# Performance work log

Hardware: AMD Instinct MI355X
Metric: run time of the kernel (lower is better)

## Reference

```python
import jax, jax.numpy as jnp
import numpy as np

N_HEAD = 16
N_KV = 4
ROT = 128  # rotary_dim == head_dim
BASE = 10000
N_CTX = 1024


def make_sincos(n_ctx, rotary_dim, base):
    # GPT-NeoX style (rotary_adjacent_pairs=False): freq repeated twice
    pos = jnp.arange(n_ctx, dtype=jnp.float32)
    dim = jnp.arange(rotary_dim // 2, dtype=jnp.float32)
    freq = jnp.float32(base) ** (dim / (rotary_dim / 2))
    freq = jnp.tile(freq, 2)  # [rotary_dim]
    angles = pos[:, None] / freq[None, :]  # [n_ctx, rotary_dim]
    return jnp.sin(angles), jnp.cos(angles)


def setup_inputs() -> dict:
    key = jax.random.key(0)
    ks = jax.random.split(key, 5)
    B, T, C = 8, 1024, 2048
    r = N_HEAD // N_KV
    Ckv = C // r
    s = 0.02
    x = jax.random.normal(ks[0], (B, T, C), jnp.float32)
    wq = jax.random.normal(ks[1], (C, C), jnp.float32) * s
    wk = jax.random.normal(ks[2], (C, Ckv), jnp.float32) * s
    wv = jax.random.normal(ks[3], (C, Ckv), jnp.float32) * s
    wo = jax.random.normal(ks[4], (C, C), jnp.float32) * s
    sin, cos = make_sincos(N_CTX, ROT, BASE)
    return dict(x=x, wq=wq, wk=wk, wv=wv, wo=wo, sin=sin, cos=cos)


def _rope(x, sin, cos):
    # x: [B, H, T, hd]; rotary applied to first ROT dims (here ROT == hd)
    T = x.shape[2]
    n = ROT // 2
    x_rot = x[..., :ROT]
    x_pass = x[..., ROT:]
    # rotate_every_two (NeoX style): [x0..x_{n-1}, x_n..] -> [-x_n.., x0..]
    x_flip = jnp.concatenate([-x_rot[..., n:], x_rot[..., :n]], axis=-1)
    c = cos[None, None, :T, :]
    s = sin[None, None, :T, :]
    x_rotated = x_rot * c + x_flip * s
    return jnp.concatenate([x_rotated, x_pass], axis=-1)


def reference(x, wq, wk, wv, wo, sin, cos):
    B, T, C = x.shape
    H = N_HEAD
    hd = C // H
    r = H // N_KV
    q = (x @ wq).reshape(B, T, H, hd).transpose(0, 2, 1, 3)  # [B,H,T,hd]
    # Original: repeat_interleave along seq dim then view(B,T,H,hd).
    # Equivalent to tiling the kv channel vector r times per position.
    k = jnp.tile(x @ wk, (1, 1, r)).reshape(B, T, H, hd).transpose(0, 2, 1, 3)
    v = jnp.tile(x @ wv, (1, 1, r)).reshape(B, T, H, hd).transpose(0, 2, 1, 3)
    q = _rope(q, sin, cos)
    k = _rope(k, sin, cos)
    att = jnp.einsum('bhqd,bhkd->bhqk', q, k) / jnp.sqrt(jnp.float32(hd))
    causal = jnp.tril(jnp.ones((T, T), dtype=bool))
    att = jnp.where(causal[None, None], att, -jnp.inf)
    att = jax.nn.softmax(att, axis=-1)
    y = jnp.einsum('bhqk,bhkd->bhqd', att, v)
    y = y.transpose(0, 2, 1, 3).reshape(B, T, C)
    return y @ wo
```

## Files before the change

### kernel.cpp

```cpp
#include <hip/hip_runtime.h>

typedef __attribute__((ext_vector_type(8))) short short8;
typedef __attribute__((ext_vector_type(4))) float f32x4;

#define B_    8
#define T_    1024
#define C_    2048
#define H_    16
#define HKV_  4
#define HD_   128
#define M_    8192
#define NQKV_ 3072
#define KDIM_ 2048

__device__ __forceinline__ unsigned short f2bf(float f) {
  unsigned u = __float_as_uint(f);
  u += 0x7FFF + ((u >> 16) & 1);
  return (unsigned short)(u >> 16);
}
__device__ __forceinline__ float bf2f(unsigned short h) {
  return __uint_as_float(((unsigned)h) << 16);
}

__device__ __forceinline__ void async16(const unsigned short* g, unsigned short* l) {
  __builtin_amdgcn_global_load_lds(
      (const unsigned int __attribute__((address_space(1)))*)g,
      (unsigned int __attribute__((address_space(3)))*)l,
      16, 0, 0);
}

__global__ __launch_bounds__(256) void cvt_bf16_kernel(const float* __restrict__ in,
                                                       unsigned short* __restrict__ out) {
  int idx = blockIdx.x * 256 + threadIdx.x;
  float4 v = ((const float4*)in)[idx];
  ushort4 o;
  o.x = f2bf(v.x); o.y = f2bf(v.y); o.z = f2bf(v.z); o.w = f2bf(v.w);
  ((ushort4*)out)[idx] = o;
}

__global__ __launch_bounds__(256) void tpose_f32_bf16(const float* __restrict__ in,
                                                      unsigned short* __restrict__ out,
                                                      int Cc, int ldo) {
  __shared__ unsigned short tile[32][33];
  int c0 = blockIdx.x * 32, r0 = blockIdx.y * 32;
  int tx = threadIdx.x, ty = threadIdx.y;
#pragma unroll
  for (int j = 0; j < 4; j++)
    tile[ty + j * 8][tx] = f2bf(in[(size_t)(r0 + ty + j * 8) * Cc + c0 + tx]);
  __syncthreads();
#pragma unroll
  for (int j = 0; j < 4; j++)
    out[(size_t)(c0 + ty + j * 8) * ldo + r0 + tx] = tile[tx][ty + j * 8];
}

__global__ __launch_bounds__(256) void vtpose(const unsigned short* __restrict__ qkv,
                                              unsigned short* __restrict__ vt) {
  __shared__ unsigned short tile[32][33];
  int b = blockIdx.z;
  int c0 = blockIdx.x * 32, t0 = blockIdx.y * 32;
  int tx = threadIdx.x, ty = threadIdx.y;
  const unsigned short* src = qkv + (size_t)b * T_ * NQKV_ + 2560;
#pragma unroll
  for (int j = 0; j < 4; j++)
    tile[ty + j * 8][tx] = src[(size_t)(t0 + ty + j * 8) * NQKV_ + c0 + tx];
  __syncthreads();
  unsigned short* dst = vt + (size_t)b * 512 * T_;
#pragma unroll
  for (int j = 0; j < 4; j++)
    dst[(size_t)(c0 + ty + j * 8) * T_ + t0 + tx] = tile[tx][ty + j * 8];
}

__global__ __launch_bounds__(256) void rope_kernel(const unsigned short* __restrict__ qkv,
                                                   const float* __restrict__ sinp,
                                                   const float* __restrict__ cosp,
                                                   unsigned short* __restrict__ qatt,
                                                   unsigned short* __restrict__ katt) {
  int m = blockIdx.x;
  int b = m >> 10, t = m & 1023;
  int tid = threadIdx.x;
  int d = tid & 63;
  const unsigned short* row = qkv + (size_t)m * NQKV_;
  float c0 = cosp[t * 128 + d], s0 = sinp[t * 128 + d];
  float c1 = cosp[t * 128 + d + 64], s1 = sinp[t * 128 + d + 64];
#pragma unroll
  for (int h0 = 0; h0 < 16; h0 += 4) {
    int h = h0 + (tid >> 6);
    float x0 = bf2f(row[h * 128 + d]);
    float x1 = bf2f(row[h * 128 + d + 64]);
    size_t o = ((size_t)(b * 16 + h) * 1024 + t) * 128 + d;
    qatt[o]      = f2bf(x0 * c0 - x1 * s0);
    qatt[o + 64] = f2bf(x1 * c1 + x0 * s1);
  }
  {
    int kh = tid >> 6;
    float x0 = bf2f(row[2048 + kh * 128 + d]);
    float x1 = bf2f(row[2048 + kh * 128 + d + 64]);
    size_t o = ((size_t)(b * 4 + kh) * 1024 + t) * 128 + d;
    katt[o]      = f2bf(x0 * c0 - x1 * s0);
    katt[o + 64] = f2bf(x1 * c1 + x0 * s1);
  }
}

template <int OUTF32>
__global__ __launch_bounds__(512, 2) void gemm_v2(const unsigned short* __restrict__ A,
                                                  const unsigned short* __restrict__ BT,
                                                  void* __restrict__ Cout, int N) {
  __shared__ __align__(16) unsigned short lA[2][256 * 64];
  __shared__ __align__(16) unsigned short lB[2][128 * 64];
  const int K = KDIM_;
  int tid = threadIdx.x;
  int lane = tid & 63;
  int w = tid >> 6;
  int quad = lane >> 4, l16 = lane & 15;
  int wm = w >> 1, wn = w & 1;
  int gx = gridDim.x;
  int nwg = gx * gridDim.y;
  int lin = blockIdx.y * gx + blockIdx.x;
  int cpx = nwg >> 3;
  int swz = (lin & 7) * cpx + (lin >> 3);
  int bm = swz / gx, bn = swz % gx;
  const unsigned short* Ab = A + (size_t)bm * 256 * K;
  const unsigned short* Bb = BT + (size_t)bn * 128 * K;
  int klin = (tid & 7) * 8;
  int arow[4], acol[4];
#pragma unroll
  for (int j = 0; j < 4; j++) {
    int r = (j * 512 + tid) >> 3;
    arow[j] = r;
    acol[j] = klin ^ (((r >> 2) & 3) * 16);
  }
  int brow[2], bcol[2];
#pragma unroll
  for (int j = 0; j < 2; j++) {
    int r = (j * 512 + tid) >> 3;
    brow[j] = r;
    bcol[j] = klin ^ (((r >> 2) & 3) * 16);
  }
  const int rsw = ((l16 >> 2) & 3) * 16;
  f32x4 acc[4][4] = {};
#pragma unroll
  for (int j = 0; j < 4; j++)
    async16(Ab + (size_t)arow[j] * K + acol[j], &lA[0][(j * 512 + tid) * 8]);
#pragma unroll
  for (int j = 0; j < 2; j++)
    async16(Bb + (size_t)brow[j] * K + bcol[j], &lB[0][(j * 512 + tid) * 8]);
  asm volatile("s_waitcnt vmcnt(0)" ::: "memory");
  __builtin_amdgcn_s_barrier();
  int cur = 0;
  for (int kt = 0; kt < 32; kt++) {
    const unsigned short* pA = lA[cur];
    const unsigned short* pB = lB[cur];
    short8 af[2][2], bfr[4][2];
#pragma unroll
    for (int mt = 0; mt < 2; mt++)
#pragma unroll
      for (int ks = 0; ks < 2; ks++)
        af[mt][ks] = *(const short8*)&pA[(wm * 64 + mt * 16 + l16) * 64 +
                                         ((ks * 32 + quad * 8) ^ rsw)];
#pragma unroll
    for (int nt = 0; nt < 4; nt++)
#pragma unroll
      for (int ks = 0; ks < 2; ks++)
        bfr[nt][ks] = *(const short8*)&pB[(wn * 64 + nt * 16 + l16) * 64 +
                                          ((ks * 32 + quad * 8) ^ rsw)];
    if (kt < 31) {
      int k0 = (kt + 1) * 64;
#pragma unroll
      for (int j = 0; j < 4; j++)
        async16(Ab + (size_t)arow[j] * K + k0 + acol[j], &lA[cur ^ 1][(j * 512 + tid) * 8]);
#pragma unroll
      for (int j = 0; j < 2; j++)
        async16(Bb + (size_t)brow[j] * K + k0 + bcol[j], &lB[cur ^ 1][(j * 512 + tid) * 8]);
    }
    __builtin_amdgcn_s_barrier();
    __builtin_amdgcn_s_setprio(1);
#pragma unroll
    for (int mt = 0; mt < 2; mt++)
#pragma unroll
      for (int nt = 0; nt < 4; nt++)
#pragma unroll
        for (int ks = 0; ks < 2; ks++)
          acc[mt][nt] = __builtin_amdgcn_mfma_f32_16x16x32_bf16(af[mt][ks], bfr[nt][ks],
                                                                acc[mt][nt], 0, 0, 0);
    __builtin_amdgcn_s_setprio(0);
    __builtin_amdgcn_s_barrier();
    short8 ag[2][2];
#pragma unroll
    for (int mt = 0; mt < 2; mt++)
#pragma unroll
      for (int ks = 0; ks < 2; ks++)
        ag[mt][ks] = *(const short8*)&pA[(wm * 64 + (mt + 2) * 16 + l16) * 64 +
                                         ((ks * 32 + quad * 8) ^ rsw)];
    __builtin_amdgcn_s_setprio(1);
#pragma unroll
    for (int mt = 0; mt < 2; mt++)
#pragma unroll
      for (int nt = 0; nt < 4; nt++)
#pragma unroll
        for (int ks = 0; ks < 2; ks++)
          acc[mt + 2][nt] = __builtin_amdgcn_mfma_f32_16x16x32_bf16(ag[mt][ks], bfr[nt][ks],
                                                                    acc[mt + 2][nt], 0, 0, 0);
    __builtin_amdgcn_s_setprio(0);
    asm volatile("s_waitcnt vmcnt(0)" ::: "memory");
    __builtin_amdgcn_s_barrier();
    cur ^= 1;
  }
#pragma unroll
  for (int mt = 0; mt < 4; mt++) {
#pragma unroll
    for (int nt = 0; nt < 4; nt++) {
      int n = bn * 128 + wn * 64 + nt * 16 + l16;
#pragma unroll
      for (int r = 0; r < 4; r++) {
        int m = bm * 256 + wm * 64 + mt * 16 + quad * 4 + r;
        if (OUTF32)
          ((float*)Cout)[(size_t)m * N + n] = acc[mt][nt][r];
        else
          ((unsigned short*)Cout)[(size_t)m * N + n] = f2bf(acc[mt][nt][r]);
      }
    }
  }
}

__global__ __launch_bounds__(256, 2) void attn_kernel(const unsigned short* __restrict__ Q,
                                                      const unsigned short* __restrict__ Km,
                                                      const unsigned short* __restrict__ Vt,
                                                      unsigned short* __restrict__ Y) {
  __shared__ __align__(16) unsigned short lK[2][8192];
  __shared__ __align__(16) unsigned short lV[2][8192];
  __shared__ __align__(16) unsigned short lP[4608];
  int tid = threadIdx.x;
  int lane = tid & 63, w = tid >> 6;
  int quad = lane >> 4, l16 = lane & 15;
  int pq = blockIdx.x;
  int bh = blockIdx.y;
  int b = bh >> 4, h = bh & 15, kh = h & 3;
  const unsigned short* Kb = Km + (size_t)(b * 4 + kh) * T_ * 128;
  const unsigned short* Vb = Vt + (size_t)(b * 4 + kh) * 128 * T_;
  const float sc = 0.12751744690989f;
  unsigned short* pb = &lP[w * 1152];
  const int sw = (l16 & 3) * 8;

  int krow[4], kcol[4], vrow[4], vcol[4];
#pragma unroll
  for (int j = 0; j < 4; j++) {
    int i = tid + j * 256;
    int tq = (i & 3) ^ ((i >> 2) & 3);
    krow[j] = (i >> 2) & 63;
    kcol[j] = (i >> 8) * 32 + tq * 8;
    vrow[j] = (i >> 2) & 127;
    vcol[j] = (i >> 9) * 32 + tq * 8;
  }

  for (int ph = 0; ph < 2; ph++) {
    int qt = ph ? pq : 7 - pq;
    int qrow0 = qt * 128 + w * 32;
    const unsigned short* Qb = Q + ((size_t)bh * T_ + qrow0) * 128;
    short8 qf[2][4];
#pragma unroll
    for (int mt = 0; mt < 2; mt++)
#pragma unroll
      for (int ks = 0; ks < 4; ks++)
        qf[mt][ks] = *(const short8*)&Qb[(mt * 16 + l16) * 128 + ks * 32 + quad * 8];
    f32x4 o[2][8] = {};
    float m_r[2][4], l_r[2][4];
#pragma unroll
    for (int mt = 0; mt < 2; mt++)
#pragma unroll
      for (int r = 0; r < 4; r++) {
        m_r[mt][r] = -1e30f;
        l_r[mt][r] = 0.f;
      }
    int ntile = 2 * qt + 2;

    if (ph) __syncthreads();
#pragma unroll
    for (int j = 0; j < 4; j++)
      async16(Kb + (size_t)krow[j] * 128 + kcol[j], &lK[0][(tid + j * 256) * 8]);
#pragma unroll
    for (int j = 0; j < 4; j++)
      async16(Vb + (size_t)vrow[j] * T_ + vcol[j], &lV[0][(tid + j * 256) * 8]);
    asm volatile("s_waitcnt vmcnt(0)" ::: "memory");
    __syncthreads();

    int cur = 0;
    for (int kt = 0; kt < ntile; kt++) {
      int n0 = kt * 64;
      if (kt + 1 < ntile) {
        int n1 = n0 + 64;
#pragma unroll
        for (int j = 0; j < 4; j++)
          async16(Kb + (size_t)(n1 + krow[j]) * 128 + kcol[j], &lK[cur ^ 1][(tid + j * 256) * 8]);
#pragma unroll
        for (int j = 0; j < 4; j++)
          async16(Vb + (size_t)vrow[j] * T_ + n1 + vcol[j], &lV[cur ^ 1][(tid + j * 256) * 8]);
      }
      const unsigned short* lKc = lK[cur];
      const unsigned short* lVc = lV[cur];
      f32x4 s[2][4] = {};
      __builtin_amdgcn_s_setprio(1);
#pragma unroll
      for (int ct = 0; ct < 4; ct++) {
        short8 kf[4];
#pragma unroll
        for (int ks = 0; ks < 4; ks++)
          kf[ks] = *(const short8*)&lKc[ks * 2048 + (ct * 16 + l16) * 32 + (quad * 8 ^ sw)];
#pragma unroll
        for (int ks = 0; ks < 4; ks++) {
          s[0][ct] = __builtin_amdgcn_mfma_f32_16x16x32_bf16(qf[0][ks], kf[ks], s[0][ct], 0, 0, 0);
          s[1][ct] = __builtin_amdgcn_mfma_f32_16x16x32_bf16(qf[1][ks], kf[ks], s[1][ct], 0, 0, 0);
        }
      }
      __builtin_amdgcn_s_setprio(0);
      if (kt >= 2 * qt) {
#pragma unroll
        for (int mt = 0; mt < 2; mt++)
#pragma unroll
          for (int ct = 0; ct < 4; ct++) {
            int n = n0 + ct * 16 + l16;
#pragma unroll
            for (int r = 0; r < 4; r++) {
              int q = qrow0 + mt * 16 + quad * 4 + r;
              if (n > q) s[mt][ct][r] = -1e30f;
            }
          }
      }
      float alpha[2][4], msc[2][4];
#pragma unroll
      for (int mt = 0; mt < 2; mt++)
#pragma unroll
        for (int r = 0; r < 4; r++) {
          float v = fmaxf(fmaxf(s[mt][0][r], s[mt][1][r]), fmaxf(s[mt][2][r], s[mt][3][r]));
#pragma unroll
          for (int off = 1; off < 16; off <<= 1)
            v = fmaxf(v, __shfl_xor(v, off));
          float mn = fmaxf(m_r[mt][r], v);
          alpha[mt][r] = exp2f((m_r[mt][r] - mn) * sc);
          m_r[mt][r] = mn;
          msc[mt][r] = mn * sc;
        }
#pragma unroll
      for (int mt = 0; mt < 2; mt++)
#pragma unroll
        for (int ct = 0; ct < 4; ct++)
#pragma unroll
          for (int r = 0; r < 4; r++)
            s[mt][ct][r] = exp2f(fmaf(s[mt][ct][r], sc, -msc[mt][r]));
#pragma unroll
      for (int ct = 0; ct < 4; ct++)
#pragma unroll
        for (int r = 0; r < 4; r++)
          pb[(quad * 4 + r) * 72 + ct * 16 + l16] = f2bf(s[0][ct][r]);
#pragma unroll
      for (int mt = 0; mt < 2; mt++)
#pragma unroll
        for (int r = 0; r < 4; r++)
          l_r[mt][r] = l_r[mt][r] * alpha[mt][r] +
                       (s[mt][0][r] + s[mt][1][r]) + (s[mt][2][r] + s[mt][3][r]);
      bool needr = false;
#pragma unroll
      for (int mt = 0; mt < 2; mt++)
#pragma unroll
        for (int r = 0; r < 4; r++)
          needr |= (alpha[mt][r] != 1.0f);
      if (__any(needr)) {
#pragma unroll
        for (int mt = 0; mt < 2; mt++)
#pragma unroll
          for (int dt = 0; dt < 8; dt++)
#pragma unroll
            for (int r = 0; r < 4; r++)
              o[mt][dt][r] *= alpha[mt][r];
      }
      __builtin_amdgcn_s_waitcnt(0xC07F);
      short8 pa0[2];
#pragma unroll
      for (int ks2 = 0; ks2 < 2; ks2++)
        pa0[ks2] = *(const short8*)&pb[l16 * 72 + ks2 * 32 + quad * 8];
      __builtin_amdgcn_s_waitcnt(0xC07F);
      asm volatile("" ::: "memory");
#pragma unroll
      for (int ct = 0; ct < 4; ct++)
#pragma unroll
        for (int r = 0; r < 4; r++)
          pb[(quad * 4 + r) * 72 + ct * 16 + l16] = f2bf(s[1][ct][r]);
      __builtin_amdgcn_s_waitcnt(0xC07F);
      short8 pa1[2];
#pragma unroll
      for (int ks2 = 0; ks2 < 2; ks2++)
        pa1[ks2] = *(const short8*)&pb[l16 * 72 + ks2 * 32 + quad * 8];
      __builtin_amdgcn_s_setprio(1);
#pragma unroll
      for (int dt = 0; dt < 8; dt++) {
#pragma unroll
        for (int ks2 = 0; ks2 < 2; ks2++) {
          short8 vf = *(const short8*)&lVc[ks2 * 4096 + (dt * 16 + l16) * 32 + (quad * 8 ^ sw)];
          o[0][dt] = __builtin_amdgcn_mfma_f32_16x16x32_bf16(pa0[ks2], vf, o[0][dt], 0, 0, 0);
          o[1][dt] = __builtin_amdgcn_mfma_f32_16x16x32_bf16(pa1[ks2], vf, o[1][dt], 0, 0, 0);
        }
      }
      __builtin_amdgcn_s_setprio(0);
      if (kt + 1 < ntile) {
        asm volatile("s_waitcnt vmcnt(0)" ::: "memory");
        __syncthreads();
        cur ^= 1;
      }
    }
#pragma unroll
    for (int mt = 0; mt < 2; mt++)
#pragma unroll
      for (int r = 0; r < 4; r++) {
        float v = l_r[mt][r];
#pragma unroll
        for (int off = 1; off < 16; off <<= 1)
          v += __shfl_xor(v, off);
        l_r[mt][r] = v;
      }
#pragma unroll
    for (int mt = 0; mt < 2; mt++)
#pragma unroll
      for (int r = 0; r < 4; r++) {
        int q = qrow0 + mt * 16 + quad * 4 + r;
        float inv = 1.f / l_r[mt][r];
        size_t base = ((size_t)(b * 1024 + q)) * 2048 + h * 128 + l16;
#pragma unroll
        for (int dt = 0; dt < 8; dt++)
          Y[base + dt * 16] = f2bf(o[mt][dt][r] * inv);
      }
  }
}

extern "C" void kernel_launch(void* const* d_in, const int* in_sizes, int n_in,
                              void* d_out, int out_size, void* d_ws, size_t ws_size,
                              hipStream_t stream) {
  const float* x    = (const float*)d_in[0];
  const float* wq   = (const float*)d_in[1];
  const float* wk   = (const float*)d_in[2];
  const float* wv   = (const float*)d_in[3];
  const float* wo   = (const float*)d_in[4];
  const float* sinp = (const float*)d_in[5];
  const float* cosp = (const float*)d_in[6];

  char* ws = (char*)d_ws;
  unsigned short* WCATT = (unsigned short*)(ws);
  unsigned short* WOT   = (unsigned short*)(ws + 12582912);
  unsigned short* XBF   = (unsigned short*)(ws + 20971520);
  unsigned short* QKV   = (unsigned short*)(ws + 54525952);
  unsigned short* KATT  = (unsigned short*)(ws + 104857600);
  unsigned short* VT    = (unsigned short*)(ws + 113246208);
  unsigned short* QATT  = XBF;
  unsigned short* Y     = QKV;

  dim3 tb(32, 8);
  cvt_bf16_kernel<<<16384, 256, 0, stream>>>(x, XBF);
  tpose_f32_bf16<<<dim3(64, 64), tb, 0, stream>>>(wq, WCATT, 2048, 2048);
  tpose_f32_bf16<<<dim3(16, 64), tb, 0, stream>>>(wk, WCATT + (size_t)2048 * 2048, 512, 2048);
  tpose_f32_bf16<<<dim3(16, 64), tb, 0, stream>>>(wv, WCATT + (size_t)2560 * 2048, 512, 2048);
  tpose_f32_bf16<<<dim3(64, 64), tb, 0, stream>>>(wo, WOT, 2048, 2048);
  gemm_v2<0><<<dim3(24, 32), 512, 0, stream>>>(XBF, WCATT, QKV, 3072);
  rope_kernel<<<8192, 256, 0, stream>>>(QKV, sinp, cosp, QATT, KATT);
  vtpose<<<dim3(16, 32, 8), tb, 0, stream>>>(QKV, VT);
  attn_kernel<<<dim3(4, 128), 256, 0, stream>>>(QATT, KATT, VT, Y);
  gemm_v2<1><<<dim3(16, 32), 512, 0, stream>>>(Y, WOT, d_out, 2048);
}
```

Before: 466.7 us.

## Restructure GEMM to 4 waves with 128x64 per-wave tiles and new LDS swizzle

The GEMM drops from 512 threads (8 waves, 64x64 per wave) to 256 threads (4 waves, 128x64 per wave), which doubles accumulator registers per wave and raises fragment reuse. The LDS XOR swizzle now uses row&7 at 8-element granularity, and the next-tile prefetch is issued before the LDS fragment reads. The mid-iteration barriers between MFMA halves are removed, leaving one barrier per k-step. In exchange, occupancy drops to one block per CU with higher register pressure, so fewer waves are available to hide latency.

```diff
diff --git a/kernel.cpp b/kernel.cpp
--- a/kernel.cpp
+++ b/kernel.cpp
@@ -102,7 +102,7 @@
 }
 
 template <int OUTF32>
-__global__ __launch_bounds__(512, 2) void gemm_v2(const unsigned short* __restrict__ A,
+__global__ __launch_bounds__(256, 1) void gemm_v3(const unsigned short* __restrict__ A,
                                                   const unsigned short* __restrict__ BT,
                                                   void* __restrict__ Cout, int N) {
   __shared__ __align__(16) unsigned short lA[2][256 * 64];
@@ -121,98 +121,84 @@
   int bm = swz / gx, bn = swz % gx;
   const unsigned short* Ab = A + (size_t)bm * 256 * K;
   const unsigned short* Bb = BT + (size_t)bn * 128 * K;
-  int klin = (tid & 7) * 8;
-  int arow[4], acol[4];
+  int arow[8], acol[8];
+#pragma unroll
+  for (int j = 0; j < 8; j++) {
+    int g = j * 256 + tid;
+    int r = g >> 3;
+    arow[j] = r;
+    acol[j] = ((g & 7) * 8) ^ ((r & 7) * 8);
+  }
+  int brow[4], bcol[4];
 #pragma unroll
   for (int j = 0; j < 4; j++) {
-    int r = (j * 512 + tid) >> 3;
-    arow[j] = r;
-    acol[j] = klin ^ (((r >> 2) & 3) * 16);
-  }
-  int brow[2], bcol[2];
-#pragma unroll
-  for (int j = 0; j < 2; j++) {
-    int r = (j * 512 + tid) >> 3;
+    int g = j * 256 + tid;
+    int r = g >> 3;
     brow[j] = r;
-    bcol[j] = klin ^ (((r >> 2) & 3) * 16);
-  }
-  const int rsw = ((l16 >> 2) & 3) * 16;
-  f32x4 acc[4][4] = {};
+    bcol[j] = ((g & 7) * 8) ^ ((r & 7) * 8);
+  }
+  const int rsw = (l16 & 7) * 8;
+  f32x4 acc[8][4] = {};
+#pragma unroll
+  for (int j = 0; j < 8; j++)
+    async16(Ab + (size_t)arow[j] * K + acol[j], &lA[0][(j * 256 + tid) * 8]);
 #pragma unroll
   for (int j = 0; j < 4; j++)
-    async16(Ab + (size_t)arow[j] * K + acol[j], &lA[0][(j * 512 + tid) * 8]);
-#pragma unroll
-  for (int j = 0; j < 2; j++)
-    async16(Bb + (size_t)brow[j] * K + bcol[j], &lB[0][(j * 512 + tid) * 8]);
+    async16(Bb + (size_t)brow[j] * K + bcol[j], &lB[0][(j * 256 + tid) * 8]);
   asm volatile("s_waitcnt vmcnt(0)" ::: "memory");
   __builtin_amdgcn_s_barrier();
   int cur = 0;
   for (int kt = 0; kt < 32; kt++) {
     const unsigned short* pA = lA[cur];
     const unsigned short* pB = lB[cur];
-    short8 af[2][2], bfr[4][2];
-#pragma unroll
-    for (int mt = 0; mt < 2; mt++)
-#pragma unroll
-      for (int ks = 0; ks < 2; ks++)
-        af[mt][ks] = *(const short8*)&pA[(wm * 64 + mt * 16 + l16) * 64 +
-                                         ((ks * 32 + quad * 8) ^ rsw)];
+    if (kt < 31) {
+      int k0 = (kt + 1) * 64;
+#pragma unroll
+      for (int j = 0; j < 8; j++)
+        async16(Ab + (size_t)arow[j] * K + k0 + acol[j], &lA[cur ^ 1][(j * 256 + tid) * 8]);
+#pragma unroll
+      for (int j = 0; j < 4; j++)
+        async16(Bb + (size_t)brow[j] * K + k0 + bcol[j], &lB[cur ^ 1][(j * 256 + tid) * 8]);
+    }
+    short8 bfr[4][2];
 #pragma unroll
     for (int nt = 0; nt < 4; nt++)
 #pragma unroll
       for (int ks = 0; ks < 2; ks++)
         bfr[nt][ks] = *(const short8*)&pB[(wn * 64 + nt * 16 + l16) * 64 +
                                           ((ks * 32 + quad * 8) ^ rsw)];
-    if (kt < 31) {
-      int k0 = (kt + 1) * 64;
-#pragma unroll
-      for (int j = 0; j < 4; j++)
-        async16(Ab + (size_t)arow[j] * K + k0 + acol[j], &lA[cur ^ 1][(j * 512 + tid) * 8]);
-#pragma unroll
-      for (int j = 0; j < 2; j++)
-        async16(Bb + (size_t)brow[j] * K + k0 + bcol[j], &lB[cur ^ 1][(j * 512 + tid) * 8]);
+#pragma unroll
+    for (int h = 0; h < 2; h++) {
+      short8 af[4][2];
+#pragma unroll
+      for (int mt = 0; mt < 4; mt++)
+#pragma unroll
+        for (int ks = 0; ks < 2; ks++)
+          af[mt][ks] = *(const short8*)&pA[(wm * 128 + (h * 4 + mt) * 16 + l16) * 64 +
+                                           ((ks * 32 + quad * 8) ^ rsw)];
+      __builtin_amdgcn_s_setprio(1);
+#pragma unroll
+      for (int mt = 0; mt < 4; mt++)
+#pragma unroll
+        for (int nt = 0; nt < 4; nt++)
+#pragma unroll
+          for (int ks = 0; ks < 2; ks++)
+            acc[h * 4 + mt][nt] = __builtin_amdgcn_mfma_f32_16x16x32_bf16(
+                af[mt][ks], bfr[nt][ks], acc[h * 4 + mt][nt], 0, 0, 0);
+      __builtin_amdgcn_s_setprio(0);
     }
-    __builtin_amdgcn_s_barrier();
-    __builtin_amdgcn_s_setprio(1);
-#pragma unroll
-    for (int mt = 0; mt < 2; mt++)
-#pragma unroll
-      for (int nt = 0; nt < 4; nt++)
-#pragma unroll
-        for (int ks = 0; ks < 2; ks++)
-          acc[mt][nt] = __builtin_amdgcn_mfma_f32_16x16x32_bf16(af[mt][ks], bfr[nt][ks],
-                                                                acc[mt][nt], 0, 0, 0);
-    __builtin_amdgcn_s_setprio(0);
-    __builtin_amdgcn_s_barrier();
-    short8 ag[2][2];
-#pragma unroll
-    for (int mt = 0; mt < 2; mt++)
-#pragma unroll
-      for (int ks = 0; ks < 2; ks++)
-        ag[mt][ks] = *(const short8*)&pA[(wm * 64 + (mt + 2) * 16 + l16) * 64 +
-                                         ((ks * 32 + quad * 8) ^ rsw)];
-    __builtin_amdgcn_s_setprio(1);
-#pragma unroll
-    for (int mt = 0; mt < 2; mt++)
-#pragma unroll
-      for (int nt = 0; nt < 4; nt++)
-#pragma unroll
-        for (int ks = 0; ks < 2; ks++)
-          acc[mt + 2][nt] = __builtin_amdgcn_mfma_f32_16x16x32_bf16(ag[mt][ks], bfr[nt][ks],
-                                                                    acc[mt + 2][nt], 0, 0, 0);
-    __builtin_amdgcn_s_setprio(0);
     asm volatile("s_waitcnt vmcnt(0)" ::: "memory");
     __builtin_amdgcn_s_barrier();
     cur ^= 1;
   }
 #pragma unroll
-  for (int mt = 0; mt < 4; mt++) {
+  for (int mt = 0; mt < 8; mt++) {
 #pragma unroll
     for (int nt = 0; nt < 4; nt++) {
       int n = bn * 128 + wn * 64 + nt * 16 + l16;
 #pragma unroll
       for (int r = 0; r < 4; r++) {
-        int m = bm * 256 + wm * 64 + mt * 16 + quad * 4 + r;
+        int m = bm * 256 + wm * 128 + mt * 16 + quad * 4 + r;
         if (OUTF32)
           ((float*)Cout)[(size_t)m * N + n] = acc[mt][nt][r];
         else
@@ -457,9 +443,9 @@
   tpose_f32_bf16<<<dim3(16, 64), tb, 0, stream>>>(wk, WCATT + (size_t)2048 * 2048, 512, 2048);
   tpose_f32_bf16<<<dim3(16, 64), tb, 0, stream>>>(wv, WCATT + (size_t)2560 * 2048, 512, 2048);
   tpose_f32_bf16<<<dim3(64, 64), tb, 0, stream>>>(wo, WOT, 2048, 2048);
-  gemm_v2<0><<<dim3(24, 32), 512, 0, stream>>>(XBF, WCATT, QKV, 3072);
+  gemm_v3<0><<<dim3(24, 32), 256, 0, stream>>>(XBF, WCATT, QKV, 3072);
   rope_kernel<<<8192, 256, 0, stream>>>(QKV, sinp, cosp, QATT, KATT);
   vtpose<<<dim3(16, 32, 8), tb, 0, stream>>>(QKV, VT);
   attn_kernel<<<dim3(4, 128), 256, 0, stream>>>(QATT, KATT, VT, Y);
-  gemm_v2<1><<<dim3(16, 32), 512, 0, stream>>>(Y, WOT, d_out, 2048);
-}
+  gemm_v3<1><<<dim3(16, 32), 256, 0, stream>>>(Y, WOT, d_out, 2048);
+}
```

Measured after the change: 568.9 us. +21.9%, slower.
